# Optimization experiments

Hardware: AMD Instinct MI355X
Metric: run time of the kernel (lower is better)

## Reference

```python
import jax, jax.numpy as jnp
import numpy as np

EMBED_DIM = 1024
NUM_HEADS = 16
HEAD_DIM = EMBED_DIM // NUM_HEADS


def setup_inputs() -> dict:
    key = jax.random.key(0)
    ks = jax.random.split(key, 9)
    B, S, E = 2, 2048, EMBED_DIM
    scale = 1.0 / np.sqrt(E)
    inp = {
        "x": jax.random.normal(ks[0], (B, S, E), dtype=jnp.float32),
        "Wq": jax.random.normal(ks[1], (E, E), dtype=jnp.float32) * scale,
        "bq": jnp.zeros((E,), dtype=jnp.float32),
        "Wk": jax.random.normal(ks[2], (E, E), dtype=jnp.float32) * scale,
        "bk": jnp.zeros((E,), dtype=jnp.float32),
        "Wv": jax.random.normal(ks[3], (E, E), dtype=jnp.float32) * scale,
        "bv": jnp.zeros((E,), dtype=jnp.float32),
        "Wo": jax.random.normal(ks[4], (E, E), dtype=jnp.float32) * scale,
        "bo": jnp.zeros((E,), dtype=jnp.float32),
    }
    return inp


def reference(x, Wq, bq, Wk, bk, Wv, bv, Wo, bo):
    B, S, E = x.shape
    H, D = NUM_HEADS, HEAD_DIM
    sm_scale = D ** (-0.5)

    def proj(W, b):
        # torch Linear: x @ W.T + b ; reshape to [B, H, S, D]
        y = jnp.einsum("bse,fe->bsf", x, W) + b
        return y.reshape(B, S, H, D).transpose(0, 2, 1, 3)

    q = proj(Wq, bq)  # [B, H, S, D]
    k = proj(Wk, bk)
    v = proj(Wv, bv)

    scores = jnp.einsum("bhqd,bhkd->bhqk", q, k) * sm_scale  # [B, H, S, S]
    attn = jax.nn.softmax(scores, axis=-1)
    o = jnp.einsum("bhqk,bhkd->bhqd", attn, v)  # [B, H, S, D]
    o = o.transpose(0, 2, 1, 3).reshape(B, S, E)
    return jnp.einsum("bse,fe->bsf", o, Wo) + bo
```

## Files before the change

### kernel.cpp

```cpp
#include <hip/hip_runtime.h>
#include <hip/hip_fp16.h>
#include <stdint.h>


typedef _Float16 f16;
typedef _Float16 f16x8 __attribute__((ext_vector_type(8)));
typedef _Float16 f16x4v __attribute__((ext_vector_type(4)));
typedef _Float16 f16x2 __attribute__((ext_vector_type(2)));
typedef float f32x4 __attribute__((ext_vector_type(4)));

#define BQ  2
#define SEQ 2048
#define EMB 1024
#define NH  16
#define HD  64
#define MM  (BQ * SEQ)

#define TR64(dst, p, OFF)                                                   \
  asm volatile("ds_read_b64_tr_b16 %0, %1 offset:" OFF                      \
               : "=v"(dst) : "v"(p) : "memory")

__device__ __forceinline__ void gld_lds16(const void* g, void* l) {
  __builtin_amdgcn_global_load_lds(
      (const __attribute__((address_space(1))) void*)g,
      (__attribute__((address_space(3))) void*)l, 16, 0, 0);
}

__device__ __forceinline__ void stage128x64(const f16* __restrict__ src,
                                            int ld, f16* lds, int tid) {
#pragma unroll
  for (int it = 0; it < 4; ++it) {
    int idx = it * 256 + tid;
    int r = idx >> 3, c = idx & 7;
    int sc = c ^ (r & 7);
    gld_lds16(src + (size_t)r * ld + sc * 8, lds + idx * 8);
  }
}

__global__ void cvt4(const float* __restrict__ src, f16* __restrict__ dst,
                     int n4) {
  int i = blockIdx.x * blockDim.x + threadIdx.x;
  if (i < n4) {
    float4 v = ((const float4*)src)[i];
    f16x4v o;
    o[0] = (f16)v.x; o[1] = (f16)v.y; o[2] = (f16)v.z; o[3] = (f16)v.w;
    ((f16x4v*)dst)[i] = o;
  }
}

__global__ void cvtW4(const float* __restrict__ s0, const float* __restrict__ s1,
                      const float* __restrict__ s2, const float* __restrict__ s3,
                      f16* __restrict__ d0, f16* __restrict__ d1,
                      f16* __restrict__ d2, f16* __restrict__ d3, int n4) {
  int i = blockIdx.x * blockDim.x + threadIdx.x;
  if (i >= n4) return;
  const float* s = (blockIdx.y == 0) ? s0 : (blockIdx.y == 1) ? s1
                   : (blockIdx.y == 2) ? s2 : s3;
  f16* d = (blockIdx.y == 0) ? d0 : (blockIdx.y == 1) ? d1
           : (blockIdx.y == 2) ? d2 : d3;
  float4 v = ((const float4*)s)[i];
  f16x4v o;
  o[0] = (f16)v.x; o[1] = (f16)v.y; o[2] = (f16)v.z; o[3] = (f16)v.w;
  ((f16x4v*)d)[i] = o;
}

template <int MODE>
__global__ __launch_bounds__(256, 2) void gemm_bt(
    const f16* __restrict__ A, const f16* __restrict__ W0,
    const f16* __restrict__ W1, const f16* __restrict__ W2,
    const float* __restrict__ b0, const float* __restrict__ b1,
    const float* __restrict__ b2, f16* __restrict__ o0, f16* __restrict__ o1,
    f16* __restrict__ o2, float* __restrict__ fo) {
  __shared__ __align__(16) f16 As[128 * 64];
  __shared__ __align__(16) f16 Bs[128 * 64];

  const int tid = threadIdx.x, lane = tid & 63, wid = tid >> 6;
  const int z = blockIdx.z;
  const f16* W = (z == 0) ? W0 : (z == 1 ? W1 : W2);
  const float* bia = (z == 0) ? b0 : (z == 1 ? b1 : b2);
  f16* outp = (z == 0) ? o0 : (z == 1 ? o1 : o2);
  const int row0 = blockIdx.x * 128, col0 = blockIdx.y * 128;
  const int wr = (wid >> 1) * 64, wc = (wid & 1) * 64;
  const int rb = lane & 15, gq = lane >> 4, sw = lane & 7;

  f32x4 acc[4][4] = {};

  for (int kt = 0; kt < EMB / 64; ++kt) {
    __syncthreads();
    stage128x64(A + (size_t)row0 * EMB + kt * 64, EMB, As, tid);
    stage128x64(W + (size_t)col0 * EMB + kt * 64, EMB, Bs, tid);
    asm volatile("s_waitcnt vmcnt(0)" ::: "memory");
    __syncthreads();
#pragma unroll
    for (int kk = 0; kk < 2; ++kk) {
      f16x8 av[4], bv[4];
#pragma unroll
      for (int f = 0; f < 4; ++f) {
        av[f] = *(const f16x8*)(As + (wr + f * 16 + rb) * 64 +
                                (((kk * 4 + gq) ^ sw) << 3));
        bv[f] = *(const f16x8*)(Bs + (wc + f * 16 + rb) * 64 +
                                (((kk * 4 + gq) ^ sw) << 3));
      }
#pragma unroll
      for (int fi = 0; fi < 4; ++fi)
#pragma unroll
        for (int fj = 0; fj < 4; ++fj)
          acc[fi][fj] = __builtin_amdgcn_mfma_f32_16x16x32_f16(
              av[fi], bv[fj], acc[fi][fj], 0, 0, 0);
    }
  }

  float bias[4];
#pragma unroll
  for (int fj = 0; fj < 4; ++fj) bias[fj] = bia[col0 + wc + fj * 16 + rb];
  const float scale = (MODE == 0 && z == 0) ? 0.18033688011112042f : 1.0f;
#pragma unroll
  for (int fi = 0; fi < 4; ++fi) {
#pragma unroll
    for (int i = 0; i < 4; ++i) {
      int row = row0 + wr + fi * 16 + gq * 4 + i;
#pragma unroll
      for (int fj = 0; fj < 4; ++fj) {
        int col = col0 + wc + fj * 16 + rb;
        float v = (acc[fi][fj][i] + bias[fj]) * scale;
        if (MODE == 0) {
          int bb = row >> 11, s = row & (SEQ - 1);
          int h = col >> 6, d = col & 63;
          outp[(((size_t)(bb * NH + h)) * SEQ + s) * HD + d] = (f16)v;
        } else {
          fo[(size_t)row * EMB + col] = v;
        }
      }
    }
  }
}

__global__ __launch_bounds__(256, 2) void attn_fwd(const f16* __restrict__ Q,
                                                   const f16* __restrict__ K,
                                                   const f16* __restrict__ V,
                                                   f16* __restrict__ O) {
  __shared__ __align__(16) f16 Ks[2][64 * 64];
  __shared__ __align__(16) f16 Vs[2][64 * 64];
  __shared__ __align__(16) f16 Pt[4][2 * 64 * 16];

  const int tid = threadIdx.x, lane = tid & 63, wid = tid >> 6;
  const int qt = blockIdx.x, bh = blockIdx.y;
  const f16* Qh = Q + (size_t)bh * SEQ * HD;
  const f16* Kh = K + (size_t)bh * SEQ * HD;
  const f16* Vh = V + (size_t)bh * SEQ * HD;
  const int q0 = qt * 128 + wid * 32;
  const int rb = lane & 15, gq = lane >> 4, sw = lane & 7;

  f16x8 aq[2][2];
#pragma unroll
  for (int rf = 0; rf < 2; ++rf)
#pragma unroll
    for (int kk = 0; kk < 2; ++kk)
      aq[rf][kk] = *(const f16x8*)(Qh + (size_t)(q0 + rf * 16 + rb) * HD +
                                   kk * 32 + gq * 8);
  asm volatile("s_waitcnt vmcnt(0)" ::: "memory");

  const int srow = tid >> 3, scol = (tid & 7) ^ (srow & 7);
  const f16* Kg0 = Kh + (size_t)srow * HD + scol * 8;

  const int L1 = tid, L2 = tid + 256;
  const int r1 = (L1 >> 1) & 63, r2 = (L2 >> 1) & 63;
  const int kv1 = (((r1 & 31) >> 2) << 3) + (r1 & 3) + ((r1 >> 5) << 2);
  const int kv2 = (((r2 & 31) >> 2) << 3) + (r2 & 3) + ((r2 >> 5) << 2);
  const f16* Vg1 = Vh + (size_t)kv1 * HD + (L1 >> 7) * 16 + (L1 & 1) * 8;
  const f16* Vg2 = Vh + (size_t)kv2 * HD + (L2 >> 7) * 16 + (L2 & 1) * 8;

  gld_lds16(Kg0,            &Ks[0][L1 * 8]);
  gld_lds16(Kg0 + 32 * HD,  &Ks[0][L2 * 8]);
  gld_lds16(Vg1,            &Vs[0][L1 * 8]);
  gld_lds16(Vg2,            &Vs[0][L2 * 8]);

  f16* Pw = &Pt[wid][0];
  f16* pwr[2][4];
#pragma unroll
  for (int rf = 0; rf < 2; ++rf)
#pragma unroll
    for (int cf = 0; cf < 4; ++cf) {
      int kv = cf * 16 + rb;
      int pr = ((kv >> 3) << 2) + (kv & 3) + ((kv & 4) << 3);
      pwr[rf][cf] = Pw + rf * 1024 + pr * 16 + gq * 4;
    }
  const __attribute__((address_space(3))) f16* ptrP =
      (const __attribute__((address_space(3))) f16*)(Pw + lane * 4);
  const __attribute__((address_space(3))) f16* ptrV0 =
      (const __attribute__((address_space(3))) f16*)(&Vs[0][0] + lane * 4);
  const __attribute__((address_space(3))) f16* ptrV1 =
      (const __attribute__((address_space(3))) f16*)(&Vs[1][0] + lane * 4);

  f16x8 ones;
#pragma unroll
  for (int j = 0; j < 8; ++j) ones[j] = (f16)1.0f;

  f32x4 oacc[2][4] = {};
  f32x4 lacc[2] = {};

  const int NT = SEQ / 64;
  for (int t = 0; t < NT; ++t) {
    __builtin_amdgcn_s_barrier();
    __builtin_amdgcn_sched_barrier(0);
    if (t + 1 < NT) {
      f16* Kn = &Ks[(t + 1) & 1][0];
      f16* Vn = &Vs[(t + 1) & 1][0];
      const size_t adv = (size_t)(t + 1) * 64 * HD;
      gld_lds16(Kg0 + adv,           Kn + L1 * 8);
      gld_lds16(Kg0 + adv + 32 * HD, Kn + L2 * 8);
      gld_lds16(Vg1 + adv,           Vn + L1 * 8);
      gld_lds16(Vg2 + adv,           Vn + L2 * 8);
      asm volatile("s_waitcnt vmcnt(4)" ::: "memory");
    } else {
      asm volatile("s_waitcnt vmcnt(0)" ::: "memory");
    }
    __builtin_amdgcn_s_barrier();
    __builtin_amdgcn_sched_barrier(0);

    const f16* Kb = &Ks[t & 1][0];
    const __attribute__((address_space(3))) f16* ptrV = (t & 1) ? ptrV1 : ptrV0;

    f32x4 s_[2][4] = {};
#pragma unroll
    for (int kk = 0; kk < 2; ++kk) {
      f16x8 bk[4];
#pragma unroll
      for (int cf = 0; cf < 4; ++cf)
        bk[cf] = *(const f16x8*)(Kb + (cf * 16 + rb) * 64 +
                                 (((kk * 4 + gq) ^ sw) << 3));
#pragma unroll
      for (int rf = 0; rf < 2; ++rf)
#pragma unroll
        for (int cf = 0; cf < 4; ++cf)
          s_[rf][cf] = __builtin_amdgcn_mfma_f32_16x16x32_f16(
              aq[rf][kk], bk[cf], s_[rf][cf], 0, 0, 0);
    }

#pragma unroll
    for (int rf = 0; rf < 2; ++rf)
#pragma unroll
      for (int cf = 0; cf < 4; ++cf) {
        float e0 = exp2f(s_[rf][cf][0]), e1 = exp2f(s_[rf][cf][1]);
        float e2 = exp2f(s_[rf][cf][2]), e3 = exp2f(s_[rf][cf][3]);
        f16x2 h01 = __builtin_bit_cast(f16x2, __builtin_amdgcn_cvt_pkrtz(e0, e1));
        f16x2 h23 = __builtin_bit_cast(f16x2, __builtin_amdgcn_cvt_pkrtz(e2, e3));
        f16x4v w;
        w[0] = h01[0]; w[1] = h01[1]; w[2] = h23[0]; w[3] = h23[1];
        *(f16x4v*)pwr[rf][cf] = w;
      }
    asm volatile("s_waitcnt lgkmcnt(0)" ::: "memory");
    __builtin_amdgcn_sched_barrier(0);

    {
      f16x4v pa, pb, pc, pd, v0a, v0b, v1a, v1b, v2a, v2b, v3a, v3b;
      TR64(pa, ptrP, "0");    TR64(pb, ptrP, "1024");
      TR64(pc, ptrP, "2048"); TR64(pd, ptrP, "3072");
      TR64(v0a, ptrV, "0");    TR64(v0b, ptrV, "1024");
      TR64(v1a, ptrV, "2048"); TR64(v1b, ptrV, "3072");
      TR64(v2a, ptrV, "4096"); TR64(v2b, ptrV, "5120");
      TR64(v3a, ptrV, "6144"); TR64(v3b, ptrV, "7168");
      asm volatile("s_waitcnt lgkmcnt(0)" ::: "memory");
      __builtin_amdgcn_sched_barrier(0);
      f16x8 bp0 = __builtin_shufflevector(pa, pb, 0, 1, 2, 3, 4, 5, 6, 7);
      f16x8 bp1 = __builtin_shufflevector(pc, pd, 0, 1, 2, 3, 4, 5, 6, 7);
      f16x8 va[4];
      va[0] = __builtin_shufflevector(v0a, v0b, 0, 1, 2, 3, 4, 5, 6, 7);
      va[1] = __builtin_shufflevector(v1a, v1b, 0, 1, 2, 3, 4, 5, 6, 7);
      va[2] = __builtin_shufflevector(v2a, v2b, 0, 1, 2, 3, 4, 5, 6, 7);
      va[3] = __builtin_shufflevector(v3a, v3b, 0, 1, 2, 3, 4, 5, 6, 7);
      lacc[0] = __builtin_amdgcn_mfma_f32_16x16x32_f16(ones, bp0, lacc[0], 0, 0, 0);
      lacc[1] = __builtin_amdgcn_mfma_f32_16x16x32_f16(ones, bp1, lacc[1], 0, 0, 0);
#pragma unroll
      for (int df = 0; df < 4; ++df) {
        oacc[0][df] = __builtin_amdgcn_mfma_f32_16x16x32_f16(va[df], bp0, oacc[0][df], 0, 0, 0);
        oacc[1][df] = __builtin_amdgcn_mfma_f32_16x16x32_f16(va[df], bp1, oacc[1][df], 0, 0, 0);
      }
    }
    {
      f16x4v pa, pb, pc, pd, v0a, v0b, v1a, v1b, v2a, v2b, v3a, v3b;
      TR64(pa, ptrP, "512");  TR64(pb, ptrP, "1536");
      TR64(pc, ptrP, "2560"); TR64(pd, ptrP, "3584");
      TR64(v0a, ptrV, "512");  TR64(v0b, ptrV, "1536");
      TR64(v1a, ptrV, "2560"); TR64(v1b, ptrV, "3584");
      TR64(v2a, ptrV, "4608"); TR64(v2b, ptrV, "5632");
      TR64(v3a, ptrV, "6656"); TR64(v3b, ptrV, "7680");
      asm volatile("s_waitcnt lgkmcnt(0)" ::: "memory");
      __builtin_amdgcn_sched_barrier(0);
      f16x8 bp0 = __builtin_shufflevector(pa, pb, 0, 1, 2, 3, 4, 5, 6, 7);
      f16x8 bp1 = __builtin_shufflevector(pc, pd, 0, 1, 2, 3, 4, 5, 6, 7);
      f16x8 va[4];
      va[0] = __builtin_shufflevector(v0a, v0b, 0, 1, 2, 3, 4, 5, 6, 7);
      va[1] = __builtin_shufflevector(v1a, v1b, 0, 1, 2, 3, 4, 5, 6, 7);
      va[2] = __builtin_shufflevector(v2a, v2b, 0, 1, 2, 3, 4, 5, 6, 7);
      va[3] = __builtin_shufflevector(v3a, v3b, 0, 1, 2, 3, 4, 5, 6, 7);
      lacc[0] = __builtin_amdgcn_mfma_f32_16x16x32_f16(ones, bp0, lacc[0], 0, 0, 0);
      lacc[1] = __builtin_amdgcn_mfma_f32_16x16x32_f16(ones, bp1, lacc[1], 0, 0, 0);
#pragma unroll
      for (int df = 0; df < 4; ++df) {
        oacc[0][df] = __builtin_amdgcn_mfma_f32_16x16x32_f16(va[df], bp0, oacc[0][df], 0, 0, 0);
        oacc[1][df] = __builtin_amdgcn_mfma_f32_16x16x32_f16(va[df], bp1, oacc[1][df], 0, 0, 0);
      }
    }
  }

  const int b = bh >> 4, h = bh & 15;
#pragma unroll
  for (int rf = 0; rf < 2; ++rf) {
    const float inv = 1.0f / lacc[rf][0];
    const int s = q0 + rf * 16 + rb;
    f16* orow = O + ((size_t)(b * SEQ + s)) * EMB + h * 64;
#pragma unroll
    for (int df = 0; df < 4; ++df) {
      f16x4v w;
#pragma unroll
      for (int i = 0; i < 4; ++i) w[i] = (f16)(oacc[rf][df][i] * inv);
      *(f16x4v*)(orow + df * 16 + gq * 4) = w;
    }
  }
}

extern "C" void kernel_launch(void* const* d_in, const int* in_sizes, int n_in,
                              void* d_out, int out_size, void* d_ws,
                              size_t ws_size, hipStream_t stream) {
  const float* x = (const float*)d_in[0];
  const float* Wq = (const float*)d_in[1];
  const float* bq = (const float*)d_in[2];
  const float* Wk = (const float*)d_in[3];
  const float* bk = (const float*)d_in[4];
  const float* Wv = (const float*)d_in[5];
  const float* bv = (const float*)d_in[6];
  const float* Wo = (const float*)d_in[7];
  const float* bo = (const float*)d_in[8];
  float* out = (float*)d_out;

  const size_t NX = (size_t)MM * EMB;
  const size_t NW = (size_t)EMB * EMB;

  f16* xh  = (f16*)d_ws;
  f16* wqh = xh + NX;
  f16* wkh = wqh + NW;
  f16* wvh = wkh + NW;
  f16* woh = wvh + NW;
  f16* Qw  = woh + NW;
  f16* Kw  = Qw + NX;
  f16* Vw  = Kw + NX;
  f16* Ow  = Vw + NX;

  cvt4<<<(int)(NX / 4 / 256), 256, 0, stream>>>(x, xh, (int)(NX / 4));
  cvtW4<<<dim3((int)(NW / 4 / 256), 4), 256, 0, stream>>>(
      Wq, Wk, Wv, Wo, wqh, wkh, wvh, woh, (int)(NW / 4));

  gemm_bt<0><<<dim3(MM / 128, EMB / 128, 3), 256, 0, stream>>>(
      xh, wqh, wkh, wvh, bq, bk, bv, Qw, Kw, Vw, nullptr);

  attn_fwd<<<dim3(SEQ / 128, BQ * NH), 256, 0, stream>>>(Qw, Kw, Vw, Ow);

  gemm_bt<1><<<dim3(MM / 128, EMB / 128, 1), 256, 0, stream>>>(
      Ow, woh, woh, woh, bo, bo, bo, nullptr, nullptr, nullptr, out);
}
```

Measured before the change: 124.1 us.

## Pre-transpose V in a separate kernel and pad P tile layout

Adds a vtrans kernel that writes V as [bh, D, S], so the attention kernel can load V tiles with the same swizzled global-to-LDS pattern as K. V fragments are then read with plain 16-byte LDS loads instead of eight ds_read_b64_tr_b16 transposed reads. The P scratch buffer gets a padded stride (80 instead of 64 elements) to reduce LDS bank conflicts on the transposed P reads. The cost is an extra kernel launch plus a full read and write of V through global memory, and more LDS for P.

```diff
diff --git a/kernel.cpp b/kernel.cpp
--- a/kernel.cpp
+++ b/kernel.cpp
@@ -135,19 +135,44 @@
   }
 }
 
+__global__ __launch_bounds__(256) void vtrans(const f16* __restrict__ V,
+                                              f16* __restrict__ Vt) {
+  __shared__ f16 T[64][72];
+  const int tid = threadIdx.x;
+  const int s0 = blockIdx.x * 64, bh = blockIdx.y;
+  const f16* Vh = V + (size_t)bh * SEQ * HD;
+  f16* Vth = Vt + (size_t)bh * HD * SEQ;
+#pragma unroll
+  for (int it = 0; it < 2; ++it) {
+    int idx = it * 256 + tid;
+    int r = idx >> 3, c0 = (idx & 7) * 8;
+    *(f16x8*)&T[r][c0] = *(const f16x8*)(Vh + (size_t)(s0 + r) * HD + c0);
+  }
+  __syncthreads();
+#pragma unroll
+  for (int it = 0; it < 2; ++it) {
+    int idx = it * 256 + tid;
+    int d = idx >> 3, sc = (idx & 7) * 8;
+    f16x8 v;
+#pragma unroll
+    for (int j = 0; j < 8; ++j) v[j] = T[sc + j][d];
+    *(f16x8*)(Vth + (size_t)d * SEQ + s0 + sc) = v;
+  }
+}
+
 __global__ __launch_bounds__(256, 2) void attn_fwd(const f16* __restrict__ Q,
                                                    const f16* __restrict__ K,
-                                                   const f16* __restrict__ V,
+                                                   const f16* __restrict__ Vt,
                                                    f16* __restrict__ O) {
   __shared__ __align__(16) f16 Ks[2][64 * 64];
   __shared__ __align__(16) f16 Vs[2][64 * 64];
-  __shared__ __align__(16) f16 Pt[4][2 * 64 * 16];
+  __shared__ __align__(16) f16 Pt[4][2560];
 
   const int tid = threadIdx.x, lane = tid & 63, wid = tid >> 6;
   const int qt = blockIdx.x, bh = blockIdx.y;
   const f16* Qh = Q + (size_t)bh * SEQ * HD;
   const f16* Kh = K + (size_t)bh * SEQ * HD;
-  const f16* Vh = V + (size_t)bh * SEQ * HD;
+  const f16* Vth = Vt + (size_t)bh * HD * SEQ;
   const int q0 = qt * 128 + wid * 32;
   const int rb = lane & 15, gq = lane >> 4, sw = lane & 7;
 
@@ -162,18 +187,12 @@
 
   const int srow = tid >> 3, scol = (tid & 7) ^ (srow & 7);
   const f16* Kg0 = Kh + (size_t)srow * HD + scol * 8;
-
-  const int L1 = tid, L2 = tid + 256;
-  const int r1 = (L1 >> 1) & 63, r2 = (L2 >> 1) & 63;
-  const int kv1 = (((r1 & 31) >> 2) << 3) + (r1 & 3) + ((r1 >> 5) << 2);
-  const int kv2 = (((r2 & 31) >> 2) << 3) + (r2 & 3) + ((r2 >> 5) << 2);
-  const f16* Vg1 = Vh + (size_t)kv1 * HD + (L1 >> 7) * 16 + (L1 & 1) * 8;
-  const f16* Vg2 = Vh + (size_t)kv2 * HD + (L2 >> 7) * 16 + (L2 & 1) * 8;
-
-  gld_lds16(Kg0,            &Ks[0][L1 * 8]);
-  gld_lds16(Kg0 + 32 * HD,  &Ks[0][L2 * 8]);
-  gld_lds16(Vg1,            &Vs[0][L1 * 8]);
-  gld_lds16(Vg2,            &Vs[0][L2 * 8]);
+  const f16* Vg0 = Vth + (size_t)srow * SEQ + scol * 8;
+
+  gld_lds16(Kg0,            &Ks[0][tid * 8]);
+  gld_lds16(Kg0 + 32 * HD,  &Ks[0][(tid + 256) * 8]);
+  gld_lds16(Vg0,            &Vs[0][tid * 8]);
+  gld_lds16(Vg0 + 32 * SEQ, &Vs[0][(tid + 256) * 8]);
 
   f16* Pw = &Pt[wid][0];
   f16* pwr[2][4];
@@ -183,14 +202,10 @@
     for (int cf = 0; cf < 4; ++cf) {
       int kv = cf * 16 + rb;
       int pr = ((kv >> 3) << 2) + (kv & 3) + ((kv & 4) << 3);
-      pwr[rf][cf] = Pw + rf * 1024 + pr * 16 + gq * 4;
+      pwr[rf][cf] = Pw + rf * 1280 + (pr >> 2) * 80 + (pr & 3) * 16 + gq * 4;
     }
   const __attribute__((address_space(3))) f16* ptrP =
-      (const __attribute__((address_space(3))) f16*)(Pw + lane * 4);
-  const __attribute__((address_space(3))) f16* ptrV0 =
-      (const __attribute__((address_space(3))) f16*)(&Vs[0][0] + lane * 4);
-  const __attribute__((address_space(3))) f16* ptrV1 =
-      (const __attribute__((address_space(3))) f16*)(&Vs[1][0] + lane * 4);
+      (const __attribute__((address_space(3))) f16*)(Pw + gq * 80 + rb * 4);
 
   f16x8 ones;
 #pragma unroll
@@ -206,11 +221,12 @@
     if (t + 1 < NT) {
       f16* Kn = &Ks[(t + 1) & 1][0];
       f16* Vn = &Vs[(t + 1) & 1][0];
-      const size_t adv = (size_t)(t + 1) * 64 * HD;
-      gld_lds16(Kg0 + adv,           Kn + L1 * 8);
-      gld_lds16(Kg0 + adv + 32 * HD, Kn + L2 * 8);
-      gld_lds16(Vg1 + adv,           Vn + L1 * 8);
-      gld_lds16(Vg2 + adv,           Vn + L2 * 8);
+      const f16* kg = Kg0 + (size_t)(t + 1) * 64 * HD;
+      const f16* vg = Vg0 + (t + 1) * 64;
+      gld_lds16(kg,            Kn + tid * 8);
+      gld_lds16(kg + 32 * HD,  Kn + (tid + 256) * 8);
+      gld_lds16(vg,            Vn + tid * 8);
+      gld_lds16(vg + 32 * SEQ, Vn + (tid + 256) * 8);
       asm volatile("s_waitcnt vmcnt(4)" ::: "memory");
     } else {
       asm volatile("s_waitcnt vmcnt(0)" ::: "memory");
@@ -219,7 +235,7 @@
     __builtin_amdgcn_sched_barrier(0);
 
     const f16* Kb = &Ks[t & 1][0];
-    const __attribute__((address_space(3))) f16* ptrV = (t & 1) ? ptrV1 : ptrV0;
+    const f16* Vb = &Vs[t & 1][0];
 
     f32x4 s_[2][4] = {};
 #pragma unroll
@@ -253,22 +269,17 @@
     __builtin_amdgcn_sched_barrier(0);
 
     {
-      f16x4v pa, pb, pc, pd, v0a, v0b, v1a, v1b, v2a, v2b, v3a, v3b;
-      TR64(pa, ptrP, "0");    TR64(pb, ptrP, "1024");
-      TR64(pc, ptrP, "2048"); TR64(pd, ptrP, "3072");
-      TR64(v0a, ptrV, "0");    TR64(v0b, ptrV, "1024");
-      TR64(v1a, ptrV, "2048"); TR64(v1b, ptrV, "3072");
-      TR64(v2a, ptrV, "4096"); TR64(v2b, ptrV, "5120");
-      TR64(v3a, ptrV, "6144"); TR64(v3b, ptrV, "7168");
+      f16x4v pa, pb, pc, pd;
+      TR64(pa, ptrP, "0");    TR64(pb, ptrP, "1280");
+      TR64(pc, ptrP, "2560"); TR64(pd, ptrP, "3840");
+      f16x8 va[4];
+#pragma unroll
+      for (int df = 0; df < 4; ++df)
+        va[df] = *(const f16x8*)(Vb + (df * 16 + rb) * 64 + ((gq ^ sw) << 3));
       asm volatile("s_waitcnt lgkmcnt(0)" ::: "memory");
       __builtin_amdgcn_sched_barrier(0);
       f16x8 bp0 = __builtin_shufflevector(pa, pb, 0, 1, 2, 3, 4, 5, 6, 7);
       f16x8 bp1 = __builtin_shufflevector(pc, pd, 0, 1, 2, 3, 4, 5, 6, 7);
-      f16x8 va[4];
-      va[0] = __builtin_shufflevector(v0a, v0b, 0, 1, 2, 3, 4, 5, 6, 7);
-      va[1] = __builtin_shufflevector(v1a, v1b, 0, 1, 2, 3, 4, 5, 6, 7);
-      va[2] = __builtin_shufflevector(v2a, v2b, 0, 1, 2, 3, 4, 5, 6, 7);
-      va[3] = __builtin_shufflevector(v3a, v3b, 0, 1, 2, 3, 4, 5, 6, 7);
       lacc[0] = __builtin_amdgcn_mfma_f32_16x16x32_f16(ones, bp0, lacc[0], 0, 0, 0);
       lacc[1] = __builtin_amdgcn_mfma_f32_16x16x32_f16(ones, bp1, lacc[1], 0, 0, 0);
 #pragma unroll
@@ -278,22 +289,17 @@
       }
     }
     {
-      f16x4v pa, pb, pc, pd, v0a, v0b, v1a, v1b, v2a, v2b, v3a, v3b;
-      TR64(pa, ptrP, "512");  TR64(pb, ptrP, "1536");
-      TR64(pc, ptrP, "2560"); TR64(pd, ptrP, "3584");
-      TR64(v0a, ptrV, "512");  TR64(v0b, ptrV, "1536");
-      TR64(v1a, ptrV, "2560"); TR64(v1b, ptrV, "3584");
-      TR64(v2a, ptrV, "4608"); TR64(v2b, ptrV, "5632");
-      TR64(v3a, ptrV, "6656"); TR64(v3b, ptrV, "7680");
+      f16x4v pa, pb, pc, pd;
+      TR64(pa, ptrP, "640");  TR64(pb, ptrP, "1920");
+      TR64(pc, ptrP, "3200"); TR64(pd, ptrP, "4480");
+      f16x8 va[4];
+#pragma unroll
+      for (int df = 0; df < 4; ++df)
+        va[df] = *(const f16x8*)(Vb + (df * 16 + rb) * 64 + (((4 + gq) ^ sw) << 3));
       asm volatile("s_waitcnt lgkmcnt(0)" ::: "memory");
       __builtin_amdgcn_sched_barrier(0);
       f16x8 bp0 = __builtin_shufflevector(pa, pb, 0, 1, 2, 3, 4, 5, 6, 7);
       f16x8 bp1 = __builtin_shufflevector(pc, pd, 0, 1, 2, 3, 4, 5, 6, 7);
-      f16x8 va[4];
-      va[0] = __builtin_shufflevector(v0a, v0b, 0, 1, 2, 3, 4, 5, 6, 7);
-      va[1] = __builtin_shufflevector(v1a, v1b, 0, 1, 2, 3, 4, 5, 6, 7);
-      va[2] = __builtin_shufflevector(v2a, v2b, 0, 1, 2, 3, 4, 5, 6, 7);
-      va[3] = __builtin_shufflevector(v3a, v3b, 0, 1, 2, 3, 4, 5, 6, 7);
       lacc[0] = __builtin_amdgcn_mfma_f32_16x16x32_f16(ones, bp0, lacc[0], 0, 0, 0);
       lacc[1] = __builtin_amdgcn_mfma_f32_16x16x32_f16(ones, bp1, lacc[1], 0, 0, 0);
 #pragma unroll
@@ -345,7 +351,8 @@
   f16* Qw  = woh + NW;
   f16* Kw  = Qw + NX;
   f16* Vw  = Kw + NX;
-  f16* Ow  = Vw + NX;
+  f16* Vtw = Vw + NX;
+  f16* Ow  = Vtw + NX;
 
   cvt4<<<(int)(NX / 4 / 256), 256, 0, stream>>>(x, xh, (int)(NX / 4));
   cvtW4<<<dim3((int)(NW / 4 / 256), 4), 256, 0, stream>>>(
@@ -354,7 +361,9 @@
   gemm_bt<0><<<dim3(MM / 128, EMB / 128, 3), 256, 0, stream>>>(
       xh, wqh, wkh, wvh, bq, bk, bv, Qw, Kw, Vw, nullptr);
 
-  attn_fwd<<<dim3(SEQ / 128, BQ * NH), 256, 0, stream>>>(Qw, Kw, Vw, Ow);
+  vtrans<<<dim3(SEQ / 64, BQ * NH), 256, 0, stream>>>(Vw, Vtw);
+
+  attn_fwd<<<dim3(SEQ / 128, BQ * NH), 256, 0, stream>>>(Qw, Kw, Vtw, Ow);
 
   gemm_bt<1><<<dim3(MM / 128, EMB / 128, 1), 256, 0, stream>>>(
       Ow, woh, woh, woh, bo, bo, bo, nullptr, nullptr, nullptr, out);
```

Measured after the change: 127.8 us. 1.03x slower.
